# Kernel tuning notes

Measured on AMD Instinct MI355X. Metric: run time of the kernel, lower is better.

The kernel has to match this reference:

```python
import jax, jax.numpy as jnp
import numpy as np

B, M, D, H = 2, 2048, 1024, 16
DH = D // H            # 64 head dim
FF = 2624              # GeGLU intermediate size
EPS = 1e-5
ROPE_BASE = 10000.0


def _layernorm(x, g, b):
    mu = jnp.mean(x, axis=-1, keepdims=True)
    var = jnp.mean(jnp.square(x - mu), axis=-1, keepdims=True)
    return (x - mu) * jax.lax.rsqrt(var + EPS) * g + b


def _rope_cos_sin(m, dh):
    # HF-style: inv_freq over even dims; only first dh/2 entries are used by apply_rope
    inv_freq = 1.0 / (ROPE_BASE ** (jnp.arange(0, dh, 2, dtype=jnp.float32) / dh))  # [dh/2]
    ang = jnp.arange(m, dtype=jnp.float32)[:, None] * inv_freq[None, :]             # [M, dh/2]
    return jnp.cos(ang), jnp.sin(ang)


def _apply_rope(x, c, s):
    # x: [B,H,M,dh]; c,s: [M,dh/2] broadcast over B,H. Half-split (non-interleaved) rotation.
    x1, x2 = jnp.split(x, 2, axis=-1)
    return jnp.concatenate([x1 * c - x2 * s, x1 * s + x2 * c], axis=-1)


def setup_inputs() -> dict:
    key = jax.random.key(0)
    ks = jax.random.split(key, 6)
    w = lambda k, shape: (jax.random.normal(k, shape, jnp.float32) * 0.02)
    return {
        "hidden_states": jax.random.normal(ks[0], (B, M, D), jnp.float32),
        "attention_mask": jnp.ones((B, M), jnp.int32),
        "ln1_g": jnp.ones((D,), jnp.float32),
        "ln1_b": jnp.zeros((D,), jnp.float32),
        "Wqkv_w": w(ks[1], (3 * D, D)),
        "Wqkv_b": jnp.zeros((3 * D,), jnp.float32),
        "Wo_w": w(ks[2], (D, D)),
        "ln2_g": jnp.ones((D,), jnp.float32),
        "ln2_b": jnp.zeros((D,), jnp.float32),
        "Wi_w": w(ks[3], (2 * FF, D)),
        "Wmlp_o_w": w(ks[4], (D, FF)),
    }


def reference(hidden_states, attention_mask, ln1_g, ln1_b, Wqkv_w, Wqkv_b, Wo_w,
              ln2_g, ln2_b, Wi_w, Wmlp_o_w):
    x = hidden_states                                    # [B,M,D]
    xn = _layernorm(x, ln1_g, ln1_b)
    qkv = xn @ Wqkv_w.T + Wqkv_b                         # [B,M,3D]
    qkv = qkv.reshape(B, M, 3, H, DH).transpose(0, 3, 1, 2, 4)  # [B,H,M,3,dh]
    q, k, v = qkv[..., 0, :], qkv[..., 1, :], qkv[..., 2, :]    # each [B,H,M,dh]

    c, s = _rope_cos_sin(M, DH)                          # [M, dh/2]
    q = _apply_rope(q, c, s)
    k = _apply_rope(k, c, s)

    scale = 1.0 / np.sqrt(DH)
    scores = jnp.einsum("bhmd,bhnd->bhmn", q, k) * scale  # [B,H,M,M]
    keep = (attention_mask > 0)[:, None, None, :]         # [B,1,1,M] padding mask on keys
    scores = jnp.where(keep, scores, -jnp.inf)
    p = jax.nn.softmax(scores, axis=-1)
    o = jnp.einsum("bhmn,bhnd->bhmd", p, v)               # [B,H,M,dh]

    attn_out = o.transpose(0, 2, 1, 3).reshape(B, M, D)
    x = x + attn_out @ Wo_w.T

    # ModernBERT GeGLU MLP: input, gate = Wi(x).chunk(2); Wo(gelu(input) * gate)
    xn2 = _layernorm(x, ln2_g, ln2_b)
    hg = xn2 @ Wi_w.T                                     # [B,M,2*FF]
    h_in, h_gate = jnp.split(hg, 2, axis=-1)
    x = x + (jax.nn.gelu(h_in) * h_gate) @ Wmlp_o_w.T
    return x
```

## Files before the change

### kernel.cpp

```cpp
#include <hip/hip_runtime.h>
#include <cstdint>
#include <cstddef>

using u16 = unsigned short;
using u32 = uint32_t;

typedef __attribute__((ext_vector_type(8))) short short8;
typedef __attribute__((ext_vector_type(4))) float floatx4;

#define DEVFN static __device__ __forceinline__

#define QSCALE 0.18033688011112042f

DEVFN u16 f2bf(float f) {
  u32 u = __float_as_uint(f);
  return (u16)((u + 0x7fffu + ((u >> 16) & 1u)) >> 16);
}

DEVFN float b2f(u16 u) { return __uint_as_float(((u32)u) << 16); }

DEVFN void async_load16(const void* g, const void* lds) {
  __builtin_amdgcn_global_load_lds(
      (const __attribute__((address_space(1))) u32*)(uintptr_t)g,
      (__attribute__((address_space(3))) u32*)(u32)(uintptr_t)lds,
      16, 0, 0);
}

DEVFN void cvt4(const float* __restrict__ src, u16* __restrict__ dst, int i) {
  const float4 v = ((const float4*)src)[i];
  ushort4 o;
  o.x = f2bf(v.x); o.y = f2bf(v.y); o.z = f2bf(v.z); o.w = f2bf(v.w);
  ((ushort4*)dst)[i] = o;
}

__global__ __launch_bounds__(256)
void prep_k(const float* __restrict__ Wqkv, const float* __restrict__ Wo,
            const float* __restrict__ Wi, const float* __restrict__ Wmlp,
            const float* __restrict__ hidden, const float* __restrict__ ln1g,
            const float* __restrict__ ln1b,
            u16* __restrict__ wqkv_bf, u16* __restrict__ wo_bf,
            u16* __restrict__ wi_bf, u16* __restrict__ wmlp_bf,
            float* __restrict__ ct, float* __restrict__ st, u16* __restrict__ xn) {
  const int bid = blockIdx.x;
  const int tid = threadIdx.x;
  __shared__ float red[8];
  if (bid < 256) {
    const int i = bid * 256 + tid;
    const int m = i >> 5, f = i & 31;
    const float inv = exp2f((float)f * -0.41524101186092025f);
    const float ang = (float)m * inv;
    ct[i] = cosf(ang);
    st[i] = sinf(ang);
  } else if (bid < 3328) {
    cvt4(Wqkv, wqkv_bf, (bid - 256) * 256 + tid);
  } else if (bid < 4352) {
    cvt4(Wo, wo_bf, (bid - 3328) * 256 + tid);
  } else if (bid < 9600) {
    const int i = (bid - 4352) * 256 + tid;
    const int i4 = i * 4;
    const int p = i4 >> 10, kc = i4 & 1023;
    const int g = p >> 5, c = p & 31;
    const int srow = (c < 16) ? (g * 16 + c) : (2624 + g * 16 + (c - 16));
    const float4 v = *(const float4*)(Wi + (size_t)srow * 1024 + kc);
    ushort4 o;
    o.x = f2bf(v.x); o.y = f2bf(v.y); o.z = f2bf(v.z); o.w = f2bf(v.w);
    ((ushort4*)wi_bf)[i] = o;
  } else if (bid < 12224) {
    cvt4(Wmlp, wmlp_bf, (bid - 9600) * 256 + tid);
  } else {
    const int row = bid - 12224;
    const float4 v = ((const float4*)(hidden + (size_t)row * 1024))[tid];
    float s = v.x + v.y + v.z + v.w;
    float ss = v.x * v.x + v.y * v.y + v.z * v.z + v.w * v.w;
#pragma unroll
    for (int d = 32; d > 0; d >>= 1) {
      s += __shfl_xor(s, d);
      ss += __shfl_xor(ss, d);
    }
    const int wave = tid >> 6;
    if ((tid & 63) == 0) { red[wave] = s; red[4 + wave] = ss; }
    __syncthreads();
    s = red[0] + red[1] + red[2] + red[3];
    ss = red[4] + red[5] + red[6] + red[7];
    const float mu = s * (1.f / 1024.f);
    const float var = ss * (1.f / 1024.f) - mu * mu;
    const float rr = rsqrtf(var + 1e-5f);
    const float4 gv = ((const float4*)ln1g)[tid];
    const float4 bv = ((const float4*)ln1b)[tid];
    u16* orow = xn + (size_t)row * 1024 + tid * 4;
    orow[0] = f2bf((v.x - mu) * rr * gv.x + bv.x);
    orow[1] = f2bf((v.y - mu) * rr * gv.y + bv.y);
    orow[2] = f2bf((v.z - mu) * rr * gv.z + bv.z);
    orow[3] = f2bf((v.w - mu) * rr * gv.w + bv.w);
  }
}

__global__ __launch_bounds__(256)
void red_ln_k(const float* __restrict__ resid, const u16* __restrict__ p0,
              const u16* __restrict__ p1, const u16* __restrict__ p2,
              const float* __restrict__ g, const float* __restrict__ bb,
              float* __restrict__ outx, u16* __restrict__ outn) {
  const int row = blockIdx.x;
  const int tid = threadIdx.x;
  const size_t base = (size_t)row * 1024;
  const float4 h = ((const float4*)(resid + base))[tid];
  const ushort4 a = ((const ushort4*)(p0 + base))[tid];
  const ushort4 c = ((const ushort4*)(p1 + base))[tid];
  const ushort4 d = ((const ushort4*)(p2 + base))[tid];
  float4 v;
  v.x = h.x + b2f(a.x) + b2f(c.x) + b2f(d.x);
  v.y = h.y + b2f(a.y) + b2f(c.y) + b2f(d.y);
  v.z = h.z + b2f(a.z) + b2f(c.z) + b2f(d.z);
  v.w = h.w + b2f(a.w) + b2f(c.w) + b2f(d.w);
  float s = v.x + v.y + v.z + v.w;
  float ss = v.x * v.x + v.y * v.y + v.z * v.z + v.w * v.w;
#pragma unroll
  for (int dd = 32; dd > 0; dd >>= 1) {
    s += __shfl_xor(s, dd);
    ss += __shfl_xor(ss, dd);
  }
  __shared__ float red[8];
  const int wave = tid >> 6;
  if ((tid & 63) == 0) { red[wave] = s; red[4 + wave] = ss; }
  __syncthreads();
  s = red[0] + red[1] + red[2] + red[3];
  ss = red[4] + red[5] + red[6] + red[7];
  const float mu = s * (1.f / 1024.f);
  const float var = ss * (1.f / 1024.f) - mu * mu;
  const float rr = rsqrtf(var + 1e-5f);
  ((float4*)(outx + base))[tid] = v;
  const float4 gv = ((const float4*)g)[tid];
  const float4 bv = ((const float4*)bb)[tid];
  u16* orow = outn + base + tid * 4;
  orow[0] = f2bf((v.x - mu) * rr * gv.x + bv.x);
  orow[1] = f2bf((v.y - mu) * rr * gv.y + bv.y);
  orow[2] = f2bf((v.z - mu) * rr * gv.z + bv.z);
  orow[3] = f2bf((v.w - mu) * rr * gv.w + bv.w);
}

__global__ void red_add_k(float* __restrict__ out, const u16* __restrict__ p0,
                          const u16* __restrict__ p1, const u16* __restrict__ p2,
                          const u16* __restrict__ p3) {
  const int i = blockIdx.x * 256 + threadIdx.x;
  float4 v = ((const float4*)out)[i];
  const ushort4 a = ((const ushort4*)p0)[i];
  const ushort4 c = ((const ushort4*)p1)[i];
  const ushort4 d = ((const ushort4*)p2)[i];
  const ushort4 e = ((const ushort4*)p3)[i];
  v.x += b2f(a.x) + b2f(c.x) + b2f(d.x) + b2f(e.x);
  v.y += b2f(a.y) + b2f(c.y) + b2f(d.y) + b2f(e.y);
  v.z += b2f(a.z) + b2f(c.z) + b2f(d.z) + b2f(e.z);
  v.w += b2f(a.w) + b2f(c.w) + b2f(d.w) + b2f(e.w);
  ((float4*)out)[i] = v;
}

__global__ __launch_bounds__(256)
void red_att_k(u16* __restrict__ att, const u16* __restrict__ p0,
               const float* __restrict__ li0, const float* __restrict__ li1) {
  const int i = blockIdx.x * 256 + threadIdx.x;
  const int i4 = i * 4;
  const int row = i4 >> 10;
  const int col = i4 & 1023;
  const int b = row >> 11, m = row & 2047;
  const int h = col >> 6;
  const int bhm = (b * 16 + h) * 2048 + m;
  const float rl = 1.f / (li0[bhm] + li1[bhm]);
  const ushort4 a = ((const ushort4*)p0)[i];
  const ushort4 c = ((const ushort4*)att)[i];
  ushort4 o;
  o.x = f2bf((b2f(a.x) + b2f(c.x)) * rl);
  o.y = f2bf((b2f(a.y) + b2f(c.y)) * rl);
  o.z = f2bf((b2f(a.z) + b2f(c.z)) * rl);
  o.w = f2bf((b2f(a.w) + b2f(c.w)) * rl);
  ((ushort4*)att)[i] = o;
}

DEVFN void swizzle_tile(int NT, int& tn, int& tm) {
  const int tpx = gridDim.x >> 3;
  const int p = blockIdx.x;
  const int lid = (p & 7) * tpx + (p >> 3);
  const int band = lid / (8 * NT);
  const int rem = lid - band * 8 * NT;
  tn = (rem >> 3) * 128;
  tm = (band * 8 + (rem & 7)) * 128;
}

struct EpiArgs {
  const float* bias;
  u16* q; u16* kk; u16* vt;
  u16* outbf;
  const float* ct; const float* st;
};

template <int EPI>
__global__ __launch_bounds__(256, 3)
void gemm_k(const u16* __restrict__ A, const u16* __restrict__ B, int K, int NT,
            EpiArgs ea) {
  __shared__ __align__(16) u16 sA[128 * 32];
  __shared__ __align__(16) u16 sB[128 * 32];
  int tn, tm;
  swizzle_tile(NT, tn, tm);
  const int tid = threadIdx.x;
  const int wave = tid >> 6, lane = tid & 63;
  const int quad = lane >> 4, l15 = lane & 15;
  const int wm = (wave >> 1) * 64, wn = (wave & 1) * 64;

  floatx4 acc[4][4];
#pragma unroll
  for (int i = 0; i < 4; ++i)
#pragma unroll
    for (int j = 0; j < 4; ++j) acc[i][j] = (floatx4){0.f, 0.f, 0.f, 0.f};

  const int srow = lane >> 2;
  const int skc = (lane & 3) * 8;
  const u16* sAr = sA + (wm + l15) * 32 + quad * 8;
  const u16* sBr = sB + (wn + l15) * 32 + quad * 8;

  for (int k0 = 0; k0 < K; k0 += 32) {
#pragma unroll
    for (int j = 0; j < 2; ++j) {
      const int q = wave * 2 + j;
      const int row = q * 16 + srow;
      async_load16(A + (size_t)(tm + row) * K + (k0 + skc), (const char*)sA + q * 1024);
      async_load16(B + (size_t)(tn + row) * K + (k0 + skc), (const char*)sB + q * 1024);
    }
    __syncthreads();
    short8 af[4], bfr[4];
#pragma unroll
    for (int t = 0; t < 4; ++t) af[t] = *(const short8*)(sAr + t * 512);
#pragma unroll
    for (int t = 0; t < 4; ++t) bfr[t] = *(const short8*)(sBr + t * 512);
#pragma unroll
    for (int ti = 0; ti < 4; ++ti)
#pragma unroll
      for (int tj = 0; tj < 4; ++tj)
        acc[ti][tj] = __builtin_amdgcn_mfma_f32_16x16x32_bf16(af[ti], bfr[tj], acc[ti][tj], 0, 0, 0);
    __syncthreads();
  }

  if constexpr (EPI == 0) {
    const int col0 = tn + wn;
    const int t = col0 >> 10;
    const int h = (col0 & 1023) >> 6;
    if (t == 2) {
#pragma unroll
      for (int ti = 0; ti < 4; ++ti)
#pragma unroll
        for (int r = 0; r < 4; ++r) {
          const int row = tm + wm + ti * 16 + quad * 4 + r;
          const int b = row >> 11, m = row & 2047;
          const int mp = (m & ~31) | ((m & 15) << 1) | ((m >> 4) & 1);
#pragma unroll
          for (int tj = 0; tj < 4; ++tj) {
            const int dh = tj * 16 + l15;
            const float v = acc[ti][tj][r] + ea.bias[col0 + dh];
            ea.vt[((size_t)((b * 16 + h) * 64 + dh)) * 2048 + mp] = f2bf(v);
          }
        }
    } else {
      u16* dst = (t == 0) ? ea.q : ea.kk;
      const float qs = (t == 0) ? QSCALE : 1.f;
#pragma unroll
      for (int ti = 0; ti < 4; ++ti)
#pragma unroll
        for (int r = 0; r < 4; ++r) {
          const int row = tm + wm + ti * 16 + quad * 4 + r;
          const int b = row >> 11, m = row & 2047;
          u16* drow = dst + ((size_t)(b * 16 + h) * 2048 + m) * 64;
#pragma unroll
          for (int tj = 0; tj < 2; ++tj) {
            const int i = tj * 16 + l15;
            const float x1 = acc[ti][tj][r] + ea.bias[col0 + i];
            const float x2 = acc[ti][tj + 2][r] + ea.bias[col0 + 32 + i];
            const float cs = ea.ct[m * 32 + i];
            const float sn = ea.st[m * 32 + i];
            drow[i] = f2bf((x1 * cs - x2 * sn) * qs);
            drow[32 + i] = f2bf((x1 * sn + x2 * cs) * qs);
          }
        }
    }
  } else {
#pragma unroll
    for (int ti = 0; ti < 4; ++ti)
#pragma unroll
      for (int r = 0; r < 4; ++r) {
        const int row = tm + wm + ti * 16 + quad * 4 + r;
#pragma unroll
        for (int u = 0; u < 2; ++u) {
          const float hin = acc[ti][2 * u][r];
          const float hg = acc[ti][2 * u + 1][r];
          const int a = (((tn + wn) >> 5) + u) * 16 + l15;
          const float t2 = hin + 0.044715f * hin * hin * hin;
          const float e = __builtin_amdgcn_exp2f(t2 * -2.302114768f);
          const float gl = hin * __builtin_amdgcn_rcpf(1.f + e);
          ea.outbf[(size_t)row * 2624 + a] = f2bf(gl * hg);
        }
      }
  }
}

__global__ __launch_bounds__(256, 3)
void gemm_sk4(const u16* __restrict__ A, const u16* __restrict__ B, int K, int NT,
              int kps1, int zsw, int kps2,
              u16* __restrict__ p0, u16* __restrict__ p1,
              u16* __restrict__ p2, u16* __restrict__ p3) {
  __shared__ __align__(16) u16 sA[128 * 32];
  __shared__ __align__(16) u16 sB[128 * 32];
  int tn, tm;
  swizzle_tile(NT, tn, tm);
  const int z = blockIdx.y;
  int kofs, kps;
  if (z < zsw) { kofs = z * kps1; kps = kps1; }
  else { kofs = zsw * kps1 + (z - zsw) * kps2; kps = kps2; }
  const int tid = threadIdx.x;
  const int wave = tid >> 6, lane = tid & 63;
  const int quad = lane >> 4, l15 = lane & 15;
  const int wm = (wave >> 1) * 64, wn = (wave & 1) * 64;

  floatx4 acc[4][4];
#pragma unroll
  for (int i = 0; i < 4; ++i)
#pragma unroll
    for (int j = 0; j < 4; ++j) acc[i][j] = (floatx4){0.f, 0.f, 0.f, 0.f};

  const int srow = lane >> 2;
  const int skc = (lane & 3) * 8;
  const u16* sAr = sA + (wm + l15) * 32 + quad * 8;
  const u16* sBr = sB + (wn + l15) * 32 + quad * 8;

  for (int k0 = 0; k0 < kps; k0 += 32) {
    const int kk = kofs + k0;
#pragma unroll
    for (int j = 0; j < 2; ++j) {
      const int q = wave * 2 + j;
      const int row = q * 16 + srow;
      async_load16(A + (size_t)(tm + row) * K + (kk + skc), (const char*)sA + q * 1024);
      async_load16(B + (size_t)(tn + row) * K + (kk + skc), (const char*)sB + q * 1024);
    }
    __syncthreads();
    short8 af[4], bfr[4];
#pragma unroll
    for (int t = 0; t < 4; ++t) af[t] = *(const short8*)(sAr + t * 512);
#pragma unroll
    for (int t = 0; t < 4; ++t) bfr[t] = *(const short8*)(sBr + t * 512);
#pragma unroll
    for (int ti = 0; ti < 4; ++ti)
#pragma unroll
      for (int tj = 0; tj < 4; ++tj)
        acc[ti][tj] = __builtin_amdgcn_mfma_f32_16x16x32_bf16(af[ti], bfr[tj], acc[ti][tj], 0, 0, 0);
    __syncthreads();
  }

  u16* part = (z == 0) ? p0 : (z == 1) ? p1 : (z == 2) ? p2 : p3;
#pragma unroll
  for (int ti = 0; ti < 4; ++ti)
#pragma unroll
    for (int r = 0; r < 4; ++r) {
      const int row = tm + wm + ti * 16 + quad * 4 + r;
#pragma unroll
      for (int tj = 0; tj < 4; ++tj)
        part[(size_t)row * 1024 + tn + wn + tj * 16 + l15] = f2bf(acc[ti][tj][r]);
    }
}

DEVFN void attn_stage64(const u16* __restrict__ kg, const u16* __restrict__ vtg,
                        size_t bhk, size_t bhv, int key0, int wave, int lane,
                        const u16* sK, const u16* sV) {
#pragma unroll
  for (int j = 0; j < 4; ++j) {
    const int qi = wave * 4 + j;
    if (qi < 8) {
      async_load16(kg + bhk + (size_t)(key0 + lane) * 64 + qi * 8,
                   (const char*)sK + qi * 1024);
    } else {
      const int vi = qi - 8;
      const int c = vi >> 2, kc = vi & 3;
      async_load16(vtg + bhv + (size_t)lane * 2048 + key0 + c * 32 + kc * 8,
                   (const char*)sV + vi * 1024);
    }
  }
}

__global__ __launch_bounds__(256, 3)
void attn_k(const u16* __restrict__ qg, const u16* __restrict__ kg,
            const u16* __restrict__ vtg, const int* __restrict__ mask,
            u16* __restrict__ p0g, u16* __restrict__ p1g,
            float* __restrict__ li0, float* __restrict__ li1) {
  __shared__ __align__(16) u16 sKV[2][8192];
  __shared__ __align__(16) u16 sP[4 * 16 * 40];
  const int L = blockIdx.x;
  const int xcd = L & 7, idx = L >> 3;
  const int bh = (xcd << 2) | (idx >> 5);
  const int local = idx & 31;
  const int q0 = (local >> 1) * 128;
  const int z = local & 1;
  const int keyBase = z << 10;
  const int b = bh >> 4, h = bh & 15;
  const int tid = threadIdx.x;
  const int wave = tid >> 6, lane = tid & 63;
  const int quad = lane >> 4, l15 = lane & 15;
  const size_t bhk = (size_t)bh * 2048 * 64;
  const size_t bhv = (size_t)bh * 64 * 2048;

  short8 aq[2][2];
#pragma unroll
  for (int g = 0; g < 2; ++g) {
    const u16* qptr = qg + ((size_t)bh * 2048 + q0 + wave * 32 + g * 16 + l15) * 64 + quad * 8;
    aq[g][0] = *(const short8*)qptr;
    aq[g][1] = *(const short8*)(qptr + 32);
  }

  floatx4 o[2][4];
#pragma unroll
  for (int g = 0; g < 2; ++g)
#pragma unroll
    for (int t = 0; t < 4; ++t) o[g][t] = (floatx4){0.f, 0.f, 0.f, 0.f};
  float li[2][4] = {{0.f, 0.f, 0.f, 0.f}, {0.f, 0.f, 0.f, 0.f}};
  const floatx4 z4 = {0.f, 0.f, 0.f, 0.f};

  attn_stage64(kg, vtg, bhk, bhv, keyBase, wave, lane, sKV[0], sKV[0] + 4096);
  __syncthreads();

  int buf = 0;
  for (int kt = 0; kt < 16; ++kt) {
    const u16* sK = sKV[buf];
    const u16* sV = sKV[buf] + 4096;
    const int key0 = keyBase + kt * 64;
    if (kt < 15) {
      attn_stage64(kg, vtg, bhk, bhv, key0 + 64, wave, lane,
                   sKV[buf ^ 1], sKV[buf ^ 1] + 4096);
    }
    float mbc[4];
#pragma unroll
    for (int tj = 0; tj < 4; ++tj)
      mbc[tj] = (mask[b * 2048 + key0 + tj * 16 + l15] > 0) ? 0.f : -1e30f;
    const float msum = mbc[0] + mbc[1] + mbc[2] + mbc[3];
    const bool allv = __all(msum == 0.f);

#pragma unroll
    for (int g = 0; g < 2; ++g) {
      floatx4 sacc[4];
      __builtin_amdgcn_s_setprio(1);
#pragma unroll
      for (int tj = 0; tj < 4; ++tj) {
        const short8 b0 = *(const short8*)(sK + quad * 512 + (tj * 16 + l15) * 8);
        const short8 b1 = *(const short8*)(sK + (4 + quad) * 512 + (tj * 16 + l15) * 8);
        sacc[tj] = __builtin_amdgcn_mfma_f32_16x16x32_bf16(aq[g][0], b0, z4, 0, 0, 0);
        sacc[tj] = __builtin_amdgcn_mfma_f32_16x16x32_bf16(aq[g][1], b1, sacc[tj], 0, 0, 0);
      }
      __builtin_amdgcn_s_setprio(0);

      if (allv) {
#pragma unroll
        for (int r = 0; r < 4; ++r) {
          float sum = li[g][r];
#pragma unroll
          for (int tj = 0; tj < 4; ++tj) {
            const float p = __builtin_amdgcn_exp2f(sacc[tj][r]);
            sacc[tj][r] = p;
            sum += p;
          }
          li[g][r] = sum;
        }
      } else {
#pragma unroll
        for (int r = 0; r < 4; ++r) {
          float sum = li[g][r];
#pragma unroll
          for (int tj = 0; tj < 4; ++tj) {
            const float p = __builtin_amdgcn_exp2f(sacc[tj][r] + mbc[tj]);
            sacc[tj][r] = p;
            sum += p;
          }
          li[g][r] = sum;
        }
      }

#pragma unroll
      for (int c = 0; c < 2; ++c) {
        u32* pw32 = (u32*)sP + wave * 320;
#pragma unroll
        for (int r = 0; r < 4; ++r) {
          const u32 lo = __float_as_uint(sacc[c * 2][r]) + 0x8000u;
          const u32 hi = __float_as_uint(sacc[c * 2 + 1][r]) + 0x8000u;
          pw32[(quad * 4 + r) * 20 + l15] = __builtin_amdgcn_perm(hi, lo, 0x07060302);
        }
        asm volatile("s_waitcnt lgkmcnt(0)" ::: "memory");
        const short8 ap = *(const short8*)(sP + wave * 640 + l15 * 40 + quad * 8);
        __builtin_amdgcn_s_setprio(1);
#pragma unroll
        for (int tj2 = 0; tj2 < 4; ++tj2) {
          const short8 bv = *(const short8*)(sV + (c * 4 + quad) * 512 + (tj2 * 16 + l15) * 8);
          o[g][tj2] = __builtin_amdgcn_mfma_f32_16x16x32_bf16(ap, bv, o[g][tj2], 0, 0, 0);
        }
        __builtin_amdgcn_s_setprio(0);
      }
    }
    __syncthreads();
    buf ^= 1;
  }

#pragma unroll
  for (int g = 0; g < 2; ++g)
#pragma unroll
    for (int r = 0; r < 4; ++r) {
      float s = li[g][r];
      s += __shfl_xor(s, 1);
      s += __shfl_xor(s, 2);
      s += __shfl_xor(s, 4);
      s += __shfl_xor(s, 8);
      li[g][r] = s;
    }

  u16* pz = z ? p1g : p0g;
  float* lz = z ? li1 : li0;
  if (l15 == 0) {
#pragma unroll
    for (int g = 0; g < 2; ++g)
#pragma unroll
      for (int r = 0; r < 4; ++r) {
        const int m = q0 + wave * 32 + g * 16 + quad * 4 + r;
        lz[(size_t)bh * 2048 + m] = li[g][r];
      }
  }

#pragma unroll
  for (int g = 0; g < 2; ++g)
#pragma unroll
    for (int tj = 0; tj < 4; ++tj)
#pragma unroll
      for (int r = 0; r < 4; ++r) {
        const int m = q0 + wave * 32 + g * 16 + quad * 4 + r;
        pz[((size_t)b * 2048 + m) * 1024 + h * 64 + tj * 16 + l15] = f2bf(o[g][tj][r]);
      }
}

static const size_t OFF_WQKV = 0;
static const size_t OFF_WO   = 6291456;
static const size_t OFF_WI   = 8388608;
static const size_t OFF_WMLP = 19136512;
static const size_t OFF_XN   = 24510464;
static const size_t OFF_Q    = 32899072;
static const size_t OFF_K    = 41287680;
static const size_t OFF_VT   = 49676288;
static const size_t OFF_ATT  = 58064896;
static const size_t OFF_ROPE = OFF_ATT;
static const size_t WS_NEED  = 66453504;

extern "C" void kernel_launch(void* const* d_in, const int* in_sizes, int n_in,
                              void* d_out, int out_size, void* d_ws, size_t ws_size,
                              hipStream_t stream) {
  (void)in_sizes; (void)n_in; (void)out_size;
  if (ws_size < WS_NEED) return;

  const float* hidden = (const float*)d_in[0];
  const int*   mask   = (const int*)d_in[1];
  const float* ln1g   = (const float*)d_in[2];
  const float* ln1b   = (const float*)d_in[3];
  const float* Wqkv   = (const float*)d_in[4];
  const float* Wqkvb  = (const float*)d_in[5];
  const float* Wo     = (const float*)d_in[6];
  const float* ln2g   = (const float*)d_in[7];
  const float* ln2b   = (const float*)d_in[8];
  const float* Wi     = (const float*)d_in[9];
  const float* Wmlp   = (const float*)d_in[10];
  float* out = (float*)d_out;
  char* ws = (char*)d_ws;

  u16* wqkv_bf = (u16*)(ws + OFF_WQKV);
  u16* wo_bf   = (u16*)(ws + OFF_WO);
  u16* wi_bf   = (u16*)(ws + OFF_WI);
  u16* wmlp_bf = (u16*)(ws + OFF_WMLP);
  u16* xn      = (u16*)(ws + OFF_XN);
  u16* qb      = (u16*)(ws + OFF_Q);
  u16* kb      = (u16*)(ws + OFF_K);
  u16* vtb     = (u16*)(ws + OFF_VT);
  u16* att     = (u16*)(ws + OFF_ATT);
  u16* act     = (u16*)(ws + OFF_Q);
  float* ct    = (float*)(ws + OFF_ROPE);
  float* st    = (float*)(ws + OFF_ROPE + 262144);
  u16* ap0     = (u16*)(ws + OFF_XN);
  u16* ap1     = (u16*)(ws + OFF_ATT);
  float* li0   = (float*)(ws + OFF_WQKV);
  float* li1   = (float*)(ws + OFF_WQKV + 262144);
  u16* wp0     = (u16*)(ws + OFF_Q);
  u16* wp1     = (u16*)(ws + OFF_K);
  u16* wp2     = (u16*)(ws + OFF_VT);
  u16* mp0     = (u16*)(ws + OFF_XN);
  u16* mp1     = (u16*)(ws + OFF_ATT);
  u16* mp2     = (u16*)(ws + OFF_WI);
  u16* mp3     = (u16*)(ws + OFF_WQKV);

  prep_k<<<16320, 256, 0, stream>>>(Wqkv, Wo, Wi, Wmlp, hidden, ln1g, ln1b,
                                    wqkv_bf, wo_bf, wi_bf, wmlp_bf, ct, st, xn);

  EpiArgs e1 = {Wqkvb, qb, kb, vtb, nullptr, ct, st};
  gemm_k<0><<<768, 256, 0, stream>>>(xn, wqkv_bf, 1024, 24, e1);

  attn_k<<<dim3(1024), 256, 0, stream>>>(qb, kb, vtb, mask, ap0, ap1, li0, li1);
  red_att_k<<<4096, 256, 0, stream>>>(att, ap0, li0, li1);

  gemm_sk4<<<dim3(256, 3), 256, 0, stream>>>(att, wo_bf, 1024, 8, 352, 2, 320,
                                             wp0, wp1, wp2, wp2);
  red_ln_k<<<4096, 256, 0, stream>>>(hidden, wp0, wp1, wp2, ln2g, ln2b, out, xn);

  EpiArgs e3 = {nullptr, nullptr, nullptr, nullptr, act, nullptr, nullptr};
  gemm_k<2><<<1312, 256, 0, stream>>>(xn, wi_bf, 1024, 41, e3);

  gemm_sk4<<<dim3(256, 4), 256, 0, stream>>>(act, wmlp_bf, 2624, 8, 672, 2, 640,
                                             mp0, mp1, mp2, mp3);
  red_add_k<<<4096, 256, 0, stream>>>(out, mp0, mp1, mp2, mp3);
}
```

Baseline: 349.3 us.

## Compute transposed S tile so P feeds PV MFMA from registers, no LDS

Swaps the MFMA operands in the QK^T product so each lane holds the scores for one query row across keys. The softmax probabilities can then be packed straight into the A-operand registers for the PV MFMA, removing the LDS round trip and the waitcnt stall. The V-transpose permutation is changed to match the new key ordering. Row sums reduce to one per lane with fewer shuffles, and the PV MFMAs for both query groups are interleaved on a shared V load. The rare masked path now does a scalar mask load per element.

```diff
diff --git a/kernel.cpp b/kernel.cpp
--- a/kernel.cpp
+++ b/kernel.cpp
@@ -7,6 +7,7 @@
 
 typedef __attribute__((ext_vector_type(8))) short short8;
 typedef __attribute__((ext_vector_type(4))) float floatx4;
+typedef __attribute__((ext_vector_type(4))) unsigned int uintx4;
 
 #define DEVFN static __device__ __forceinline__
 
@@ -18,6 +19,11 @@
 }
 
 DEVFN float b2f(u16 u) { return __uint_as_float(((u32)u) << 16); }
+
+DEVFN u32 pkbf(float lo, float hi) {
+  return __builtin_amdgcn_perm(__float_as_uint(hi) + 0x8000u,
+                               __float_as_uint(lo) + 0x8000u, 0x07060302u);
+}
 
 DEVFN void async_load16(const void* g, const void* lds) {
   __builtin_amdgcn_global_load_lds(
@@ -249,7 +255,7 @@
         for (int r = 0; r < 4; ++r) {
           const int row = tm + wm + ti * 16 + quad * 4 + r;
           const int b = row >> 11, m = row & 2047;
-          const int mp = (m & ~31) | ((m & 15) << 1) | ((m >> 4) & 1);
+          const int mp = (m & ~31) | ((m & 12) << 1) | ((m & 16) >> 2) | (m & 3);
 #pragma unroll
           for (int tj = 0; tj < 4; ++tj) {
             const int dh = tj * 16 + l15;
@@ -387,7 +393,6 @@
             u16* __restrict__ p0g, u16* __restrict__ p1g,
             float* __restrict__ li0, float* __restrict__ li1) {
   __shared__ __align__(16) u16 sKV[2][8192];
-  __shared__ __align__(16) u16 sP[4 * 16 * 40];
   const int L = blockIdx.x;
   const int xcd = L & 7, idx = L >> 3;
   const int bh = (xcd << 2) | (idx >> 5);
@@ -415,7 +420,7 @@
   for (int g = 0; g < 2; ++g)
 #pragma unroll
     for (int t = 0; t < 4; ++t) o[g][t] = (floatx4){0.f, 0.f, 0.f, 0.f};
-  float li[2][4] = {{0.f, 0.f, 0.f, 0.f}, {0.f, 0.f, 0.f, 0.f}};
+  float li[2] = {0.f, 0.f};
   const floatx4 z4 = {0.f, 0.f, 0.f, 0.f};
 
   attn_stage64(kg, vtg, bhk, bhv, keyBase, wave, lane, sKV[0], sKV[0] + 4096);
@@ -430,13 +435,9 @@
       attn_stage64(kg, vtg, bhk, bhv, key0 + 64, wave, lane,
                    sKV[buf ^ 1], sKV[buf ^ 1] + 4096);
     }
-    float mbc[4];
-#pragma unroll
-    for (int tj = 0; tj < 4; ++tj)
-      mbc[tj] = (mask[b * 2048 + key0 + tj * 16 + l15] > 0) ? 0.f : -1e30f;
-    const float msum = mbc[0] + mbc[1] + mbc[2] + mbc[3];
-    const bool allv = __all(msum == 0.f);
-
+    const bool allv = __all(mask[b * 2048 + key0 + lane] > 0);
+
+    short8 pa[2][2];
 #pragma unroll
     for (int g = 0; g < 2; ++g) {
       floatx4 sacc[4];
@@ -445,83 +446,77 @@
       for (int tj = 0; tj < 4; ++tj) {
         const short8 b0 = *(const short8*)(sK + quad * 512 + (tj * 16 + l15) * 8);
         const short8 b1 = *(const short8*)(sK + (4 + quad) * 512 + (tj * 16 + l15) * 8);
-        sacc[tj] = __builtin_amdgcn_mfma_f32_16x16x32_bf16(aq[g][0], b0, z4, 0, 0, 0);
-        sacc[tj] = __builtin_amdgcn_mfma_f32_16x16x32_bf16(aq[g][1], b1, sacc[tj], 0, 0, 0);
+        sacc[tj] = __builtin_amdgcn_mfma_f32_16x16x32_bf16(b0, aq[g][0], z4, 0, 0, 0);
+        sacc[tj] = __builtin_amdgcn_mfma_f32_16x16x32_bf16(b1, aq[g][1], sacc[tj], 0, 0, 0);
       }
       __builtin_amdgcn_s_setprio(0);
 
       if (allv) {
-#pragma unroll
-        for (int r = 0; r < 4; ++r) {
-          float sum = li[g][r];
-#pragma unroll
-          for (int tj = 0; tj < 4; ++tj) {
+        float sum = li[g];
+#pragma unroll
+        for (int tj = 0; tj < 4; ++tj)
+#pragma unroll
+          for (int r = 0; r < 4; ++r) {
             const float p = __builtin_amdgcn_exp2f(sacc[tj][r]);
             sacc[tj][r] = p;
             sum += p;
           }
-          li[g][r] = sum;
-        }
+        li[g] = sum;
       } else {
-#pragma unroll
-        for (int r = 0; r < 4; ++r) {
-          float sum = li[g][r];
-#pragma unroll
-          for (int tj = 0; tj < 4; ++tj) {
-            const float p = __builtin_amdgcn_exp2f(sacc[tj][r] + mbc[tj]);
+        float sum = li[g];
+#pragma unroll
+        for (int tj = 0; tj < 4; ++tj)
+#pragma unroll
+          for (int r = 0; r < 4; ++r) {
+            const int key = key0 + tj * 16 + quad * 4 + r;
+            const float mb = (mask[b * 2048 + key] > 0) ? 0.f : -1e30f;
+            const float p = __builtin_amdgcn_exp2f(sacc[tj][r] + mb);
             sacc[tj][r] = p;
             sum += p;
           }
-          li[g][r] = sum;
-        }
+        li[g] = sum;
       }
 
 #pragma unroll
       for (int c = 0; c < 2; ++c) {
-        u32* pw32 = (u32*)sP + wave * 320;
-#pragma unroll
-        for (int r = 0; r < 4; ++r) {
-          const u32 lo = __float_as_uint(sacc[c * 2][r]) + 0x8000u;
-          const u32 hi = __float_as_uint(sacc[c * 2 + 1][r]) + 0x8000u;
-          pw32[(quad * 4 + r) * 20 + l15] = __builtin_amdgcn_perm(hi, lo, 0x07060302);
-        }
-        asm volatile("s_waitcnt lgkmcnt(0)" ::: "memory");
-        const short8 ap = *(const short8*)(sP + wave * 640 + l15 * 40 + quad * 8);
-        __builtin_amdgcn_s_setprio(1);
-#pragma unroll
-        for (int tj2 = 0; tj2 < 4; ++tj2) {
-          const short8 bv = *(const short8*)(sV + (c * 4 + quad) * 512 + (tj2 * 16 + l15) * 8);
-          o[g][tj2] = __builtin_amdgcn_mfma_f32_16x16x32_bf16(ap, bv, o[g][tj2], 0, 0, 0);
-        }
-        __builtin_amdgcn_s_setprio(0);
+        uintx4 w;
+        w.x = pkbf(sacc[2 * c][0], sacc[2 * c][1]);
+        w.y = pkbf(sacc[2 * c][2], sacc[2 * c][3]);
+        w.z = pkbf(sacc[2 * c + 1][0], sacc[2 * c + 1][1]);
+        w.w = pkbf(sacc[2 * c + 1][2], sacc[2 * c + 1][3]);
+        pa[g][c] = __builtin_bit_cast(short8, w);
       }
+    }
+
+#pragma unroll
+    for (int c = 0; c < 2; ++c) {
+      __builtin_amdgcn_s_setprio(1);
+#pragma unroll
+      for (int tj2 = 0; tj2 < 4; ++tj2) {
+        const short8 bv = *(const short8*)(sV + (c * 4 + quad) * 512 + (tj2 * 16 + l15) * 8);
+        o[0][tj2] = __builtin_amdgcn_mfma_f32_16x16x32_bf16(pa[0][c], bv, o[0][tj2], 0, 0, 0);
+        o[1][tj2] = __builtin_amdgcn_mfma_f32_16x16x32_bf16(pa[1][c], bv, o[1][tj2], 0, 0, 0);
+      }
+      __builtin_amdgcn_s_setprio(0);
     }
     __syncthreads();
     buf ^= 1;
   }
 
 #pragma unroll
-  for (int g = 0; g < 2; ++g)
-#pragma unroll
-    for (int r = 0; r < 4; ++r) {
-      float s = li[g][r];
-      s += __shfl_xor(s, 1);
-      s += __shfl_xor(s, 2);
-      s += __shfl_xor(s, 4);
-      s += __shfl_xor(s, 8);
-      li[g][r] = s;
-    }
+  for (int g = 0; g < 2; ++g) {
+    float s = li[g];
+    s += __shfl_xor(s, 16);
+    s += __shfl_xor(s, 32);
+    li[g] = s;
+  }
 
   u16* pz = z ? p1g : p0g;
   float* lz = z ? li1 : li0;
-  if (l15 == 0) {
+  if (lane < 16) {
 #pragma unroll
     for (int g = 0; g < 2; ++g)
-#pragma unroll
-      for (int r = 0; r < 4; ++r) {
-        const int m = q0 + wave * 32 + g * 16 + quad * 4 + r;
-        lz[(size_t)bh * 2048 + m] = li[g][r];
-      }
+      lz[(size_t)bh * 2048 + q0 + wave * 32 + g * 16 + l15] = li[g];
   }
 
 #pragma unroll
```

After: 345.4 us. Within noise of the previous version (-1.1%).
